# Performance work log

Measured on AMD Instinct MI355X. Metric: run time of the kernel, lower is better.

The kernel has to match this reference:

```python
import jax, jax.numpy as jnp
import numpy as np

EPS = 1e-8

def setup_inputs() -> dict:
    key = jax.random.key(0)
    k1, k2, k3, k4, k5 = jax.random.split(key, 5)
    B, C_in, C_out, H, W, S, K = 16, 128, 128, 128, 128, 512, 3
    return {
        "x": jax.random.normal(k1, (B, C_in, H, W), dtype=jnp.float32),
        "style": jax.random.normal(k2, (B, S), dtype=jnp.float32),
        "weight": jax.random.normal(k3, (1, C_out, C_in, K, K), dtype=jnp.float32),
        "mod_w": jax.random.normal(k4, (C_in, S), dtype=jnp.float32) * 0.05,
        "mod_b": jax.random.normal(k5, (C_in,), dtype=jnp.float32) * 0.05,
    }

def _modulated_weights(style, weight, mod_w, mod_b):
    # style: [B, S] -> s: [B, C_in]
    s = style @ mod_w.T + mod_b
    # w: [B, C_out, C_in, K, K]
    w = weight * s[:, None, :, None, None]
    # demodulation: rsqrt of sum of squares over (C_in, K, K)
    decoef = jax.lax.rsqrt(jnp.sum(w * w, axis=(2, 3, 4)) + EPS)  # [B, C_out]
    return w * decoef[:, :, None, None, None]

def _conv_one(xi, wi):
    # xi: [C_in, H, W], wi: [C_out, C_in, K, K]; 'SAME' padding (K//2)
    out = jax.lax.conv_general_dilated(
        xi[None], wi,
        window_strides=(1, 1), padding="SAME",
        dimension_numbers=("NCHW", "OIHW", "NCHW"))
    return out[0]

def reference(x, style, weight, mod_w, mod_b):
    w = _modulated_weights(style, weight, mod_w, mod_b)  # [B, C_out, C_in, K, K]
    # per-sample conv (equivalent to groups=B grouped conv in torch)
    return jax.vmap(_conv_one)(x, w)  # [B, C_out, H, W]
```

## Files before the change

### kernel.cpp

```cpp
#include <hip/hip_runtime.h>
#include <hip/hip_bf16.h>


#define Bn 16
#define Cc 128
#define HW 128
#define Sv 512

typedef __bf16 bf16x8 __attribute__((ext_vector_type(8)));
typedef float f32x4 __attribute__((ext_vector_type(4)));
typedef unsigned short ushort8 __attribute__((ext_vector_type(8)));

static __device__ __forceinline__ unsigned short bf16bits(float f) {
    return __builtin_bit_cast(unsigned short, __float2bfloat16(f));
}

static __device__ __forceinline__ void gl_lds16(const void* g, void* l) {
    __builtin_amdgcn_global_load_lds(
        (const __attribute__((address_space(1))) unsigned int*)g,
        (__attribute__((address_space(3))) unsigned int*)l, 16, 0, 0);
}

__global__ __launch_bounds__(64) void k_style(const float* __restrict__ style,
                                              const float* __restrict__ mod_w,
                                              const float* __restrict__ mod_b,
                                              float* __restrict__ s_out) {
    int b = blockIdx.x >> 7, ci = blockIdx.x & 127;
    int lane = threadIdx.x;
    const float* st = style + (size_t)b * Sv;
    const float* mw = mod_w + (size_t)ci * Sv;
    float acc = 0.f;
#pragma unroll
    for (int k = 0; k < Sv; k += 64)
        acc += st[k + lane] * mw[k + lane];
#pragma unroll
    for (int off = 32; off > 0; off >>= 1)
        acc += __shfl_down(acc, off, 64);
    if (lane == 0) s_out[b * Cc + ci] = acc + mod_b[ci];
}

__global__ __launch_bounds__(128) void k_mod(const float* __restrict__ weight,
                                             const float* __restrict__ s,
                                             __hip_bfloat16* __restrict__ wsW) {
    int b = blockIdx.x >> 7;
    int co = blockIdx.x & 127;
    int ci = threadIdx.x;
    float sv = s[b * Cc + ci];
    const float* wp = weight + ((size_t)co * Cc + ci) * 9;
    float wv[9];
    float ss = 0.f;
#pragma unroll
    for (int j = 0; j < 9; j++) {
        wv[j] = wp[j] * sv;
        ss += wv[j] * wv[j];
    }
    __shared__ float red[128];
    red[ci] = ss;
    __syncthreads();
    for (int s2 = 64; s2 > 0; s2 >>= 1) {
        if (ci < s2) red[ci] += red[ci + s2];
        __syncthreads();
    }
    float dec = rsqrtf(red[0] + 1e-8f);
    int pos = ((((ci >> 3) ^ (co & 7)) << 3) | (ci & 7));
#pragma unroll
    for (int j = 0; j < 9; j++) {
        wsW[(((size_t)b * 9 + j) * Cc + co) * Cc + pos] = __float2bfloat16(wv[j] * dec);
    }
}

__global__ __launch_bounds__(512, 2) void k_conv(const float* __restrict__ x,
                                                 const __hip_bfloat16* __restrict__ wsW,
                                                 float* __restrict__ out) {
    __shared__ __align__(16) __bf16 Xs[4 * 128 * 128];
    __shared__ __align__(16) __bf16 Ws[128 * 128];

    int bx0 = blockIdx.x;
    int bx = (bx0 & 7) * 128 + (bx0 >> 3);
    int b = bx >> 6;
    int h0 = (bx & 63) << 1;

    int t = threadIdx.x;
    int lane = t & 63;
    int wv = t >> 6;
    int m2 = wv >> 2;
    int th = (wv >> 1) & 1;
    int n2 = wv & 1;
    int l15 = lane & 15, quad = lane >> 4;

    f32x4 acc[4][4] = {};

    const float* xb = x + (size_t)b * (Cc * HW * HW);
    const __hip_bfloat16* wbase = wsW + (size_t)b * 9 * (Cc * Cc);

    for (int j = 0; j < 4; j++) {
        int hp = h0 - 1 + j;
        bool ok = (unsigned)hp < (unsigned)HW;
        const float* xr = xb + (size_t)hp * HW;
#pragma unroll
        for (int c = 0; c < 4; c++) {
            int id = c * 512 + t;
            int w = id & 127;
            int g = id >> 7;
            ushort8 pk = {};
            if (ok) {
                const float* p = xr + (size_t)g * 8 * (HW * HW) + w;
#pragma unroll
                for (int e = 0; e < 8; e++)
                    pk[e] = bf16bits(p[(size_t)e * (HW * HW)]);
            }
            *(bf16x8*)(&Xs[j * 16384 + w * 128 + ((g ^ (w & 7)) << 3)]) =
                __builtin_bit_cast(bf16x8, pk);
        }
    }

    for (int kh = 0; kh < 3; kh++) {
        int xbuf = (kh + th) * 16384;
        for (int kw = 0; kw < 3; kw++) {
            __syncthreads();
            const __hip_bfloat16* wsrc = wbase + (size_t)(kh * 3 + kw) * (Cc * Cc);
#pragma unroll
            for (int c = 0; c < 4; c++) {
                int chunk = wv * 4 + c;
                gl_lds16(wsrc + chunk * 512 + lane * 8, &Ws[chunk * 512]);
            }
            __syncthreads();
#pragma unroll
            for (int ks = 0; ks < 4; ks++) {
                int kg = ks * 4 + quad;
                bf16x8 a[4], bb[4];
#pragma unroll
                for (int mi = 0; mi < 4; mi++) {
                    int co = m2 * 64 + mi * 16 + l15;
                    a[mi] = *(const bf16x8*)(&Ws[co * 128 + ((kg ^ (co & 7)) << 3)]);
                }
#pragma unroll
                for (int ni = 0; ni < 4; ni++) {
                    int xr = n2 * 64 + ni * 16 + l15 + kw - 1;
                    int xrc = min(127, max(0, xr));
                    bf16x8 v = *(const bf16x8*)(
                        &Xs[xbuf + xrc * 128 + ((kg ^ (xrc & 7)) << 3)]);
                    if (xr != xrc) v = (bf16x8){};
                    bb[ni] = v;
                }
#pragma unroll
                for (int mi = 0; mi < 4; mi++)
#pragma unroll
                    for (int ni = 0; ni < 4; ni++)
                        acc[mi][ni] = __builtin_amdgcn_mfma_f32_16x16x32_bf16(
                            a[mi], bb[ni], acc[mi][ni], 0, 0, 0);
            }
        }
    }

    int h = h0 + th;
    float* ob = out + (size_t)b * (Cc * HW * HW) + (size_t)h * HW;
#pragma unroll
    for (int mi = 0; mi < 4; mi++) {
#pragma unroll
        for (int ni = 0; ni < 4; ni++) {
            int w = n2 * 64 + ni * 16 + l15;
#pragma unroll
            for (int r = 0; r < 4; r++) {
                int co = m2 * 64 + mi * 16 + quad * 4 + r;
                ob[(size_t)co * (HW * HW) + w] = acc[mi][ni][r];
            }
        }
    }
}

extern "C" void kernel_launch(void* const* d_in, const int* in_sizes, int n_in,
                              void* d_out, int out_size, void* d_ws, size_t ws_size,
                              hipStream_t stream) {
    const float* x      = (const float*)d_in[0];
    const float* style  = (const float*)d_in[1];
    const float* weight = (const float*)d_in[2];
    const float* mod_w  = (const float*)d_in[3];
    const float* mod_b  = (const float*)d_in[4];
    float* out = (float*)d_out;

    float* s_ws = (float*)d_ws;
    __hip_bfloat16* wsW = (__hip_bfloat16*)((char*)d_ws + 8192);

    k_style<<<Bn * Cc, 64, 0, stream>>>(style, mod_w, mod_b, s_ws);
    k_mod<<<Bn * Cc, 128, 0, stream>>>(weight, s_ws, wsW);
    k_conv<<<Bn * (HW / 2), 512, 0, stream>>>(x, wsW, out);
}
```

Baseline: 313.4 us.

## Load weight MFMA fragments directly from global, drop LDS weight staging

The modulation kernel now writes demodulated weights in a pre-swizzled MFMA fragment layout, so each lane's A-operand is one contiguous 16-byte global load. The conv kernel no longer stages weights through LDS and drops the two barriers per tap, loading all 16 A fragments per tap into registers. This frees 32KB of LDS and removes sync stalls, at the cost of more VGPRs and exposed global/L2 load latency for the weights. Each block still reads the same per-batch weights.

Result: faster. 302.3 us (-3.5%).

```diff
diff --git a/kernel.cpp b/kernel.cpp
--- a/kernel.cpp
+++ b/kernel.cpp
@@ -13,12 +13,6 @@
 
 static __device__ __forceinline__ unsigned short bf16bits(float f) {
     return __builtin_bit_cast(unsigned short, __float2bfloat16(f));
-}
-
-static __device__ __forceinline__ void gl_lds16(const void* g, void* l) {
-    __builtin_amdgcn_global_load_lds(
-        (const __attribute__((address_space(1))) unsigned int*)g,
-        (__attribute__((address_space(3))) unsigned int*)l, 16, 0, 0);
 }
 
 __global__ __launch_bounds__(64) void k_style(const float* __restrict__ style,
@@ -62,10 +56,13 @@
         __syncthreads();
     }
     float dec = rsqrtf(red[0] + 1e-8f);
-    int pos = ((((ci >> 3) ^ (co & 7)) << 3) | (ci & 7));
+    int frag = ((co >> 6) << 4) | (((co >> 4) & 3) << 2) | (ci >> 5);
+    int lane = (((ci >> 3) & 3) << 4) | (co & 15);
+    int e = ci & 7;
 #pragma unroll
     for (int j = 0; j < 9; j++) {
-        wsW[(((size_t)b * 9 + j) * Cc + co) * Cc + pos] = __float2bfloat16(wv[j] * dec);
+        wsW[(((size_t)b * 9 + j) * 32 + frag) * 512 + lane * 8 + e] =
+            __float2bfloat16(wv[j] * dec);
     }
 }
 
@@ -73,7 +70,6 @@
                                                  const __hip_bfloat16* __restrict__ wsW,
                                                  float* __restrict__ out) {
     __shared__ __align__(16) __bf16 Xs[4 * 128 * 128];
-    __shared__ __align__(16) __bf16 Ws[128 * 128];
 
     int bx0 = blockIdx.x;
     int bx = (bx0 & 7) * 128 + (bx0 >> 3);
@@ -91,7 +87,6 @@
     f32x4 acc[4][4] = {};
 
     const float* xb = x + (size_t)b * (Cc * HW * HW);
-    const __hip_bfloat16* wbase = wsW + (size_t)b * 9 * (Cc * Cc);
 
     for (int j = 0; j < 4; j++) {
         int hp = h0 - 1 + j;
@@ -113,27 +108,27 @@
                 __builtin_bit_cast(bf16x8, pk);
         }
     }
+    __syncthreads();
 
+    const __hip_bfloat16* wb2 =
+        wsW + ((size_t)b * 9) * (32 * 512) + (size_t)(m2 * 16) * 512 + lane * 8;
+
+#pragma unroll
     for (int kh = 0; kh < 3; kh++) {
         int xbuf = (kh + th) * 16384;
+#pragma unroll
         for (int kw = 0; kw < 3; kw++) {
-            __syncthreads();
-            const __hip_bfloat16* wsrc = wbase + (size_t)(kh * 3 + kw) * (Cc * Cc);
+            const __hip_bfloat16* af = wb2 + (size_t)(kh * 3 + kw) * (32 * 512);
+            bf16x8 a[4][4];
 #pragma unroll
-            for (int c = 0; c < 4; c++) {
-                int chunk = wv * 4 + c;
-                gl_lds16(wsrc + chunk * 512 + lane * 8, &Ws[chunk * 512]);
-            }
-            __syncthreads();
+            for (int ks = 0; ks < 4; ks++)
+#pragma unroll
+                for (int mi = 0; mi < 4; mi++)
+                    a[ks][mi] = *(const bf16x8*)(af + (size_t)(mi * 4 + ks) * 512);
 #pragma unroll
             for (int ks = 0; ks < 4; ks++) {
                 int kg = ks * 4 + quad;
-                bf16x8 a[4], bb[4];
-#pragma unroll
-                for (int mi = 0; mi < 4; mi++) {
-                    int co = m2 * 64 + mi * 16 + l15;
-                    a[mi] = *(const bf16x8*)(&Ws[co * 128 + ((kg ^ (co & 7)) << 3)]);
-                }
+                bf16x8 bb[4];
 #pragma unroll
                 for (int ni = 0; ni < 4; ni++) {
                     int xr = n2 * 64 + ni * 16 + l15 + kw - 1;
@@ -148,7 +143,7 @@
 #pragma unroll
                     for (int ni = 0; ni < 4; ni++)
                         acc[mi][ni] = __builtin_amdgcn_mfma_f32_16x16x32_bf16(
-                            a[mi], bb[ni], acc[mi][ni], 0, 0, 0);
+                            a[ks][mi], bb[ni], acc[mi][ni], 0, 0, 0);
             }
         }
     }
```

## Double-buffer per-half-tap weight tiles in MFMA fragment layout

Applied to the files above, without the earlier changes.

The modulation kernel now writes demodulated weights pre-arranged in MFMA A-fragment order, staged through shared memory so the global stores are 16-byte vectorised. The conv kernel splits each tap into two K-halves and double-buffers 16 KB weight slices, prefetching the next slice while computing the current one. This replaces two barriers per tap with one barrier per half-tap and lets A fragments be read with contiguous lane loads. It also raises MFMA wave priority and limits the boundary-zeroing check to the edge fragments. The cost is more barrier rounds and smaller prefetch granularity.

Result: slower. 322.3 us (+2.8%).

```diff
diff --git a/kernel.cpp b/kernel.cpp
--- a/kernel.cpp
+++ b/kernel.cpp
@@ -55,6 +55,7 @@
         ss += wv[j] * wv[j];
     }
     __shared__ float red[128];
+    __shared__ __align__(16) __bf16 wo[9 * 128];
     red[ci] = ss;
     __syncthreads();
     for (int s2 = 64; s2 > 0; s2 >>= 1) {
@@ -62,10 +63,21 @@
         __syncthreads();
     }
     float dec = rsqrtf(red[0] + 1e-8f);
-    int pos = ((((ci >> 3) ^ (co & 7)) << 3) | (ci & 7));
-#pragma unroll
-    for (int j = 0; j < 9; j++) {
-        wsW[(((size_t)b * 9 + j) * Cc + co) * Cc + pos] = __float2bfloat16(wv[j] * dec);
+#pragma unroll
+    for (int j = 0; j < 9; j++)
+        wo[j * 128 + ci] = __float2bfloat16(wv[j] * dec);
+    __syncthreads();
+    int fragbase = ((co >> 6) << 4) | (((co >> 4) & 3) << 2);
+#pragma unroll
+    for (int it = 0; it < 2; it++) {
+        int c = it * 128 + ci;
+        if (c < 144) {
+            int j = c >> 4, g = c & 15;
+            bf16x8 chunk = *(const bf16x8*)(&wo[j * 128 + g * 8]);
+            size_t off = (((size_t)b * 9 + j) * 32 + fragbase + (g >> 2)) * 512 +
+                         (size_t)(((g & 3) << 4) | (co & 15)) * 8;
+            *(bf16x8*)(wsW + off) = chunk;
+        }
     }
 }
 
@@ -73,7 +85,7 @@
                                                  const __hip_bfloat16* __restrict__ wsW,
                                                  float* __restrict__ out) {
     __shared__ __align__(16) __bf16 Xs[4 * 128 * 128];
-    __shared__ __align__(16) __bf16 Ws[128 * 128];
+    __shared__ __align__(16) __bf16 Ws[2][16 * 512];
 
     int bx0 = blockIdx.x;
     int bx = (bx0 & 7) * 128 + (bx0 >> 3);
@@ -83,16 +95,25 @@
     int t = threadIdx.x;
     int lane = t & 63;
     int wv = t >> 6;
-    int m2 = wv >> 2;
-    int th = (wv >> 1) & 1;
-    int n2 = wv & 1;
+    int wave_m = wv >> 2;
+    int wave_n = wv & 3;
+    int hsub = wave_n >> 1;
+    int wbase = (wave_n & 1) << 6;
     int l15 = lane & 15, quad = lane >> 4;
 
     f32x4 acc[4][4] = {};
 
     const float* xb = x + (size_t)b * (Cc * HW * HW);
-    const __hip_bfloat16* wbase = wsW + (size_t)b * 9 * (Cc * Cc);
-
+    const __hip_bfloat16* wtb = wsW + (size_t)b * 9 * (32 * 512) + (size_t)lane * 8;
+
+#pragma unroll
+    for (int q = 0; q < 2; q++) {
+        int fb = wv * 2 + q;
+        int f = ((fb >> 3) << 4) + (((fb >> 1) & 3) << 2) + (fb & 1);
+        gl_lds16(wtb + (size_t)f * 512, &Ws[0][fb * 512]);
+    }
+
+#pragma unroll
     for (int j = 0; j < 4; j++) {
         int hp = h0 - 1 + j;
         bool ok = (unsigned)hp < (unsigned)HW;
@@ -113,56 +134,64 @@
                 __builtin_bit_cast(bf16x8, pk);
         }
     }
-
-    for (int kh = 0; kh < 3; kh++) {
-        int xbuf = (kh + th) * 16384;
-        for (int kw = 0; kw < 3; kw++) {
-            __syncthreads();
-            const __hip_bfloat16* wsrc = wbase + (size_t)(kh * 3 + kw) * (Cc * Cc);
-#pragma unroll
-            for (int c = 0; c < 4; c++) {
-                int chunk = wv * 4 + c;
-                gl_lds16(wsrc + chunk * 512 + lane * 8, &Ws[chunk * 512]);
-            }
-            __syncthreads();
-#pragma unroll
-            for (int ks = 0; ks < 4; ks++) {
-                int kg = ks * 4 + quad;
-                bf16x8 a[4], bb[4];
-#pragma unroll
-                for (int mi = 0; mi < 4; mi++) {
-                    int co = m2 * 64 + mi * 16 + l15;
-                    a[mi] = *(const bf16x8*)(&Ws[co * 128 + ((kg ^ (co & 7)) << 3)]);
+    __syncthreads();
+
+#pragma unroll
+    for (int p = 0; p < 18; p++) {
+        const int tap = p >> 1, ht = p & 1, buf = p & 1;
+        const int kh = tap / 3, kw = tap % 3;
+        if (p < 17) {
+            const int ntap = (p + 1) >> 1, nht = (p + 1) & 1, nbuf = (p + 1) & 1;
+#pragma unroll
+            for (int q = 0; q < 2; q++) {
+                int fb = wv * 2 + q;
+                int f = ((fb >> 3) << 4) + (((fb >> 1) & 3) << 2) + 2 * nht + (fb & 1);
+                gl_lds16(wtb + ((size_t)ntap * 32 + f) * 512, &Ws[nbuf][fb * 512]);
+            }
+        }
+        const int jimg = hsub + kh;
+#pragma unroll
+        for (int jj = 0; jj < 2; jj++) {
+            const int ks = ht * 2 + jj;
+            int kg = ks * 4 + quad;
+            bf16x8 a[4], bb[4];
+#pragma unroll
+            for (int mi = 0; mi < 4; mi++)
+                a[mi] = *(const bf16x8*)(
+                    &Ws[buf][(wave_m * 8 + mi * 2 + jj) * 512 + lane * 8]);
+#pragma unroll
+            for (int ni = 0; ni < 4; ni++) {
+                int xc = wbase + ni * 16 + l15 + kw - 1;
+                int xcc = min(127, max(0, xc));
+                bf16x8 v = *(const bf16x8*)(
+                    &Xs[jimg * 16384 + xcc * 128 + ((kg ^ (xcc & 7)) << 3)]);
+                if ((kw == 0 && ni == 0) || (kw == 2 && ni == 3)) {
+                    if (xc != xcc) v = (bf16x8){};
                 }
-#pragma unroll
-                for (int ni = 0; ni < 4; ni++) {
-                    int xr = n2 * 64 + ni * 16 + l15 + kw - 1;
-                    int xrc = min(127, max(0, xr));
-                    bf16x8 v = *(const bf16x8*)(
-                        &Xs[xbuf + xrc * 128 + ((kg ^ (xrc & 7)) << 3)]);
-                    if (xr != xrc) v = (bf16x8){};
-                    bb[ni] = v;
-                }
-#pragma unroll
-                for (int mi = 0; mi < 4; mi++)
-#pragma unroll
-                    for (int ni = 0; ni < 4; ni++)
-                        acc[mi][ni] = __builtin_amdgcn_mfma_f32_16x16x32_bf16(
-                            a[mi], bb[ni], acc[mi][ni], 0, 0, 0);
-            }
-        }
-    }
-
-    int h = h0 + th;
+                bb[ni] = v;
+            }
+            __builtin_amdgcn_s_setprio(1);
+#pragma unroll
+            for (int mi = 0; mi < 4; mi++)
+#pragma unroll
+                for (int ni = 0; ni < 4; ni++)
+                    acc[mi][ni] = __builtin_amdgcn_mfma_f32_16x16x32_bf16(
+                        a[mi], bb[ni], acc[mi][ni], 0, 0, 0);
+            __builtin_amdgcn_s_setprio(0);
+        }
+        __syncthreads();
+    }
+
+    int h = h0 + hsub;
     float* ob = out + (size_t)b * (Cc * HW * HW) + (size_t)h * HW;
 #pragma unroll
     for (int mi = 0; mi < 4; mi++) {
 #pragma unroll
         for (int ni = 0; ni < 4; ni++) {
-            int w = n2 * 64 + ni * 16 + l15;
+            int w = wbase + ni * 16 + l15;
 #pragma unroll
             for (int r = 0; r < 4; r++) {
-                int co = m2 * 64 + mi * 16 + quad * 4 + r;
+                int co = wave_m * 64 + mi * 16 + quad * 4 + r;
                 ob[(size_t)co * (HW * HW) + w] = acc[mi][ni][r];
             }
         }
```
